# Kernel optimization log

Hardware: AMD Instinct MI355X
Metric: run time of the kernel (lower is better)

## Reference

```python
import jax, jax.numpy as jnp
import numpy as np

EMB = 256
HEADS = 4
HD = EMB // HEADS
BS, SZ = 4, 64


def _layernorm(x, g, b, eps=1e-5):
    mu = jnp.mean(x, axis=-1, keepdims=True)
    var = jnp.mean((x - mu) ** 2, axis=-1, keepdims=True)
    return (x - mu) * jax.lax.rsqrt(var + eps) * g + b


def setup_inputs() -> dict:
    key = jax.random.key(0)
    ks = jax.random.split(key, 12)
    s = lambda k, shape, sc: jax.random.normal(k, shape, jnp.float32) * sc
    return {
        "x": s(ks[0], (BS, EMB, SZ, SZ), 1.0),
        "ln1_g": jnp.ones((EMB,), jnp.float32),
        "ln1_b": jnp.zeros((EMB,), jnp.float32),
        "wq": s(ks[1], (HD, HD), HD ** -0.5), "bq": jnp.zeros((HD,), jnp.float32),
        "wk": s(ks[2], (HD, HD), HD ** -0.5), "bk": jnp.zeros((HD,), jnp.float32),
        "wv": s(ks[3], (HD, HD), HD ** -0.5), "bv": jnp.zeros((HD,), jnp.float32),
        "wo": s(ks[4], (EMB, EMB), EMB ** -0.5), "bo": jnp.zeros((EMB,), jnp.float32),
        "ln2_g": jnp.ones((EMB,), jnp.float32),
        "ln2_b": jnp.zeros((EMB,), jnp.float32),
        "w1": s(ks[5], (EMB, EMB), EMB ** -0.5), "b1": jnp.zeros((EMB,), jnp.float32),
        "w2": s(ks[6], (EMB, EMB), EMB ** -0.5), "b2": jnp.zeros((EMB,), jnp.float32),
    }


def reference(x, ln1_g, ln1_b, wq, bq, wk, bk, wv, bv, wo, bo, ln2_g, ln2_b, w1, b1, w2, b2):
    bs, c, sz, _ = x.shape
    seq = sz * sz
    xt = x.reshape(bs, c, seq).swapaxes(1, 2)  # [b, s, c]
    xn = _layernorm(xt, ln1_g, ln1_b)
    # split heads: [b, h, s, d]
    h = xn.reshape(bs, seq, HEADS, HD).transpose(0, 2, 1, 3)
    q = h @ wq + bq
    k = h @ wk + bk
    v = h @ wv + bv
    scores = jnp.einsum("bhqd,bhkd->bhqk", q, k) / (HD ** 0.5)
    attn = jax.nn.softmax(scores, axis=-1)
    o = jnp.einsum("bhqk,bhkd->bhqd", attn, v)
    o = o.transpose(0, 2, 1, 3).reshape(bs, seq, c)
    o = o @ wo + bo
    av = o + xt  # residual 1
    ff = _layernorm(av, ln2_g, ln2_b) @ w1 + b1
    ff = jax.nn.gelu(ff, approximate=False) @ w2 + b2
    out = ff + av  # residual 2
    return out.swapaxes(1, 2).reshape(bs, c, sz, sz)
```

## Files before the change

kernel.cpp:

```cpp
#include <hip/hip_runtime.h>
#include <hip/hip_bf16.h>
#include <cstdint>

typedef __attribute__((ext_vector_type(8))) short short8;
typedef __attribute__((ext_vector_type(4))) short short4_;
typedef __attribute__((ext_vector_type(4))) float float4_;

#define MFMA16(a,b,c)  __builtin_amdgcn_mfma_f32_16x16x32_bf16(a,b,c,0,0,0)
#define MFMA16K16(a,b,c) __builtin_amdgcn_mfma_f32_16x16x16bf16_1k(a,b,c,0,0,0)
#define EXP2(x) __builtin_amdgcn_exp2f(x)

__device__ __forceinline__ short f2bs(float f) {
    union { float f; uint32_t u; } c;
    c.f = f;
    c.u += 0x7FFF + ((c.u >> 16) & 1);
    return (short)(c.u >> 16);
}
__device__ __forceinline__ float s2f(short s) {
    union { uint32_t u; float f; } c;
    c.u = ((uint32_t)(uint16_t)s) << 16;
    return c.f;
}

static const int EMB = 256;
static const int SEQ = 4096;
static const int TOK = 16384;

#define QSCALE 0.18033688011112042f

__global__ __launch_bounds__(256) void repack_kernel(
    const float* wq, const float* wk, const float* wv,
    const float* wo, const float* w1, const float* w2,
    short* wqT, short* wkT, short* wvT, short* woT, short* w1T, short* w2T)
{
    int idx = blockIdx.x * 256 + threadIdx.x;
    if (idx < 3 * 4096) {
        int m = idx / 4096, r = idx % 4096;
        int n = r / 64, k = r % 64;
        const float* src = (m == 0) ? wq : (m == 1) ? wk : wv;
        short* dst = (m == 0) ? wqT : (m == 1) ? wkT : wvT;
        float v = src[k * 64 + n];
        if (m == 0) v *= QSCALE;
        dst[n * 64 + k] = f2bs(v);
    } else {
        int idx2 = idx - 3 * 4096;
        if (idx2 < 3 * 65536) {
            int m = idx2 / 65536, r = idx2 % 65536;
            int n = r / 256, k = r % 256;
            const float* src = (m == 0) ? wo : (m == 1) ? w1 : w2;
            short* dst = (m == 0) ? woT : (m == 1) ? w1T : w2T;
            dst[n * 256 + k] = f2bs(src[k * 256 + n]);
        }
    }
}

__global__ __launch_bounds__(64) void ln1_kernel(
    const float* x, const float* g, const float* bta,
    short* xn, short* xt)
{
    int t = blockIdx.x * 64 + threadIdx.x;
    int b = t >> 12, sp = t & 4095;
    const float* xb = x + (size_t)b * EMB * SEQ + sp;
    float sum = 0.f, ss = 0.f;
#pragma unroll 32
    for (int c = 0; c < 256; c++) {
        float v = xb[(size_t)c * SEQ];
        sum += v; ss += v * v;
    }
    float mu = sum * (1.f / 256.f);
    float var = ss * (1.f / 256.f) - mu * mu;
    float rs = rsqrtf(var + 1e-5f);
    short* xnr = xn + (size_t)t * 256;
    short* xtr = xt + (size_t)t * 256;
#pragma unroll 8
    for (int c = 0; c < 256; c += 4) {
        short4_ ra, na;
#pragma unroll
        for (int j = 0; j < 4; j++) {
            float v = xb[(size_t)(c + j) * SEQ];
            ra[j] = f2bs(v);
            na[j] = f2bs((v - mu) * rs * g[c + j] + bta[c + j]);
        }
        *(short4_*)(xtr + c) = ra;
        *(short4_*)(xnr + c) = na;
    }
}

__global__ __launch_bounds__(256) void qkv_kernel(
    const short* xn, const short* wqT, const short* wkT, const short* wvT,
    const float* bq, const float* bk, const float* bv,
    short* qo, short* ko, short* vto)
{
    int tid = threadIdx.x;
    int w = tid >> 6, lane = tid & 63, quad = lane >> 4, l15 = lane & 15;
    int m0 = blockIdx.x * 64 + w * 16;
    int row = m0 + l15;
    int bb = row >> 12;
    int s0 = (m0 & 4095) + quad * 4;

    short8 a0[4], a1[4];
#pragma unroll
    for (int h = 0; h < 4; h++) {
        a0[h] = *(const short8*)(xn + (size_t)row * 256 + h * 64 + quad * 8);
        a1[h] = *(const short8*)(xn + (size_t)row * 256 + h * 64 + 32 + quad * 8);
    }

#pragma unroll
    for (int p = 0; p < 3; p++) {
        const short* WT = (p == 0) ? wqT : (p == 1) ? wkT : wvT;
        const float* bias = (p == 0) ? bq : (p == 1) ? bk : bv;
        float bscale = (p == 0) ? QSCALE : 1.f;
#pragma unroll
        for (int nb = 0; nb < 4; nb++) {
            int col = nb * 16 + l15;
            short8 b0 = *(const short8*)(WT + col * 64 + quad * 8);
            short8 b1 = *(const short8*)(WT + col * 64 + 32 + quad * 8);
            float bvv = bias[col] * bscale;
#pragma unroll
            for (int h = 0; h < 4; h++) {
                float4_ acc = {bvv, bvv, bvv, bvv};
                acc = MFMA16(a0[h], b0, acc);
                acc = MFMA16(a1[h], b1, acc);
                size_t headbase = (size_t)(bb * 4 + h) * SEQ;
                if (p < 2) {
                    short* dst = (p == 0) ? qo : ko;
#pragma unroll
                    for (int r = 0; r < 4; r++)
                        dst[(headbase + s0 + r) * 64 + col] = f2bs(acc[r]);
                } else {
                    short4_ pk;
#pragma unroll
                    for (int r = 0; r < 4; r++) pk[r] = f2bs(acc[r]);
                    *(short4_*)(vto + ((size_t)(bb * 4 + h) * 64 + col) * SEQ + s0) = pk;
                }
            }
        }
    }
}

__global__ __launch_bounds__(256, 4) void flash_kernel(
    const short* q, const short* k, const short* vt,
    short* O0, short* O1, float* l0, float* l1)
{
    __shared__ short K_lds[64 * 64];
    __shared__ short V_lds[64 * 64];

    int tid = threadIdx.x;
    int w = tid >> 6, lane = tid & 63, quad = lane >> 4, l15 = lane & 15;
    int qt = blockIdx.x, bh = blockIdx.y, grp = blockIdx.z;
    int span = 64 / gridDim.z;

    const short* qb = q + (size_t)bh * SEQ * 64;
    const short* kb = k + (size_t)bh * SEQ * 64 + (size_t)grp * span * 64 * 64;
    const short* vb = vt + (size_t)bh * 64 * SEQ + grp * span * 64;

    int qrow0 = qt * 128 + w * 32 + l15;
    int qrow1 = qrow0 + 16;
    short8 qA0 = *(const short8*)(qb + (size_t)qrow0 * 64 + quad * 8);
    short8 qA1 = *(const short8*)(qb + (size_t)qrow0 * 64 + 32 + quad * 8);
    short8 qB0 = *(const short8*)(qb + (size_t)qrow1 * 64 + quad * 8);
    short8 qB1 = *(const short8*)(qb + (size_t)qrow1 * 64 + 32 + quad * 8);

    float4_ oacc0[4], oacc1[4];
#pragma unroll
    for (int md = 0; md < 4; md++) {
        oacc0[md] = {0.f, 0.f, 0.f, 0.f};
        oacc1[md] = {0.f, 0.f, 0.f, 0.f};
    }
    float li0 = 0.f, li1 = 0.f;

    int srow = tid >> 2;
    int sr7 = srow & 7;
    int c0 = tid & 3;
    int l7 = l15 & 7;

    int dcA = (c0 ^ sr7) << 3;
    int dcB = ((c0 + 4) ^ sr7) << 3;

    short8 kr0 = *(const short8*)(kb + (size_t)srow * 64 + c0 * 8);
    short8 kr1 = *(const short8*)(kb + (size_t)srow * 64 + (c0 + 4) * 8);
    short8 vr0 = *(const short8*)(vb + (size_t)srow * SEQ + c0 * 8);
    short8 vr1 = *(const short8*)(vb + (size_t)srow * SEQ + (c0 + 4) * 8);

    for (int kt = 0; kt < span; kt++) {
        __syncthreads();
        *(short8*)&K_lds[srow * 64 + dcA] = kr0;
        *(short8*)&K_lds[srow * 64 + dcB] = kr1;
        *(short8*)&V_lds[srow * 64 + dcA] = vr0;
        *(short8*)&V_lds[srow * 64 + dcB] = vr1;
        if (kt + 1 < span) {
            kr0 = *(const short8*)(kb + (size_t)((kt + 1) * 64 + srow) * 64 + c0 * 8);
            kr1 = *(const short8*)(kb + (size_t)((kt + 1) * 64 + srow) * 64 + (c0 + 4) * 8);
            vr0 = *(const short8*)(vb + (size_t)srow * SEQ + (kt + 1) * 64 + c0 * 8);
            vr1 = *(const short8*)(vb + (size_t)srow * SEQ + (kt + 1) * 64 + (c0 + 4) * 8);
        }
        asm volatile("s_waitcnt lgkmcnt(0)" ::: "memory");
        __builtin_amdgcn_s_barrier();
        asm volatile("" ::: "memory");

        float4_ s0[4], s1[4];
#pragma unroll
        for (int nb = 0; nb < 4; nb++) {
            short8 k0 = *(const short8*)&K_lds[(nb * 16 + l15) * 64 + ((quad ^ l7) << 3)];
            short8 k1 = *(const short8*)&K_lds[(nb * 16 + l15) * 64 + (((quad + 4) ^ l7) << 3)];
            float4_ a = {0.f, 0.f, 0.f, 0.f};
            a = MFMA16(k0, qA0, a);
            a = MFMA16(k1, qA1, a);
            s0[nb] = a;
            float4_ b = {0.f, 0.f, 0.f, 0.f};
            b = MFMA16(k0, qB0, b);
            b = MFMA16(k1, qB1, b);
            s1[nb] = b;
        }

        short4_ pf0[4], pf1[4];
#pragma unroll
        for (int nb = 0; nb < 4; nb++) {
            float p00 = EXP2(s0[nb][0]), p01 = EXP2(s0[nb][1]);
            float p02 = EXP2(s0[nb][2]), p03 = EXP2(s0[nb][3]);
            li0 += (p00 + p01) + (p02 + p03);
            float p10 = EXP2(s1[nb][0]), p11 = EXP2(s1[nb][1]);
            float p12 = EXP2(s1[nb][2]), p13 = EXP2(s1[nb][3]);
            li1 += (p10 + p11) + (p12 + p13);
            union { short4_ s; uint32_t u[2]; } pa, pb;
            asm("v_cvt_pk_bf16_f32 %0, %1, %2" : "=v"(pa.u[0]) : "v"(p00), "v"(p01));
            asm("v_cvt_pk_bf16_f32 %0, %1, %2" : "=v"(pa.u[1]) : "v"(p02), "v"(p03));
            asm("v_cvt_pk_bf16_f32 %0, %1, %2" : "=v"(pb.u[0]) : "v"(p10), "v"(p11));
            asm("v_cvt_pk_bf16_f32 %0, %1, %2" : "=v"(pb.u[1]) : "v"(p12), "v"(p13));
            pf0[nb] = pa.s;
            pf1[nb] = pb.s;
        }

#pragma unroll
        for (int md = 0; md < 4; md++)
#pragma unroll
            for (int nb = 0; nb < 4; nb++) {
                int c = nb * 2 + (quad >> 1);
                short4_ vf = *(const short4_*)&V_lds[(md * 16 + l15) * 64 +
                                                     ((c ^ l7) << 3) + ((quad & 1) << 2)];
                oacc0[md] = MFMA16K16(vf, pf0[nb], oacc0[md]);
                oacc1[md] = MFMA16K16(vf, pf1[nb], oacc1[md]);
            }
    }

    li0 += __shfl_xor(li0, 16);
    li0 += __shfl_xor(li0, 32);
    li1 += __shfl_xor(li1, 16);
    li1 += __shfl_xor(li1, 32);

    short* Op = grp ? O1 : O0;
    float* lp = grp ? l1 : l0;
    if (quad == 0) {
        lp[bh * 4096 + qrow0] = li0;
        lp[bh * 4096 + qrow1] = li1;
    }

    size_t ob0 = ((size_t)bh * 4096 + qrow0) * 64;
    size_t ob1 = ((size_t)bh * 4096 + qrow1) * 64;
#pragma unroll
    for (int md = 0; md < 4; md++) {
        short4_ pk0, pk1;
#pragma unroll
        for (int r = 0; r < 4; r++) {
            pk0[r] = f2bs(oacc0[md][r]);
            pk1[r] = f2bs(oacc1[md][r]);
        }
        *(short4_*)(Op + ob0 + md * 16 + quad * 4) = pk0;
        *(short4_*)(Op + ob1 + md * 16 + quad * 4) = pk1;
    }
}

__global__ __launch_bounds__(256) void combine_kernel(
    const short* O0, const short* O1, const float* l0, const float* l1,
    short* Oout, int two)
{
    int g = blockIdx.x * 256 + threadIdx.x;
    int qi = g >> 4;
    short4_ a = *(const short4_*)(O0 + (size_t)g * 4);
    float l = l0[qi];
    float4_ acc = {s2f(a[0]), s2f(a[1]), s2f(a[2]), s2f(a[3])};
    if (two) {
        short4_ b = *(const short4_*)(O1 + (size_t)g * 4);
        l += l1[qi];
#pragma unroll
        for (int j = 0; j < 4; j++) acc[j] += s2f(b[j]);
    }
    float inv = 1.f / l;
    short4_ pk;
#pragma unroll
    for (int j = 0; j < 4; j++) pk[j] = f2bs(acc[j] * inv);
    *(short4_*)(Oout + (size_t)g * 4) = pk;
}

__global__ __launch_bounds__(256) void mlp_kernel(
    const short* O,
    const short* woT, const short* w1T, const short* w2T,
    const float* bo, const float* b1, const float* b2,
    const float* g2, const float* be2,
    const short* xt, float* outf)
{
    __shared__ __align__(16) char smem[3 * 8448 + 128];
    short* av = (short*)smem;
    short* x2 = (short*)(smem + 8448);
    short* ff = (short*)(smem + 16896);
    float* stats = (float*)(smem + 25344);
    float* T = (float*)smem;

    int tid = threadIdx.x;
    int w = tid >> 6, lane = tid & 63, quad = lane >> 4, l15 = lane & 15;
    int m0 = blockIdx.x * 16;
    int n0 = w * 64;
    int arow = m0 + l15;
    int bbA = arow >> 12, spA = arow & 4095;

    float4_ acc[4];
#pragma unroll
    for (int nb = 0; nb < 4; nb++) {
        float bvv = bo[n0 + nb * 16 + l15];
        acc[nb] = {bvv, bvv, bvv, bvv};
    }
    for (int kc = 0; kc < 8; kc++) {
        int h = kc >> 1;
        int off = (kc & 1) * 32 + quad * 8;
        short8 a = *(const short8*)(O + ((size_t)(bbA * 4 + h) * 4096 + spA) * 64 + off);
#pragma unroll
        for (int nb = 0; nb < 4; nb++) {
            short8 b = *(const short8*)(woT + (size_t)(n0 + nb * 16 + l15) * 256 + kc * 32 + quad * 8);
            acc[nb] = MFMA16(a, b, acc[nb]);
        }
    }
#pragma unroll
    for (int nb = 0; nb < 4; nb++) {
        int col = n0 + nb * 16 + l15;
#pragma unroll
        for (int r = 0; r < 4; r++) {
            size_t t = (size_t)m0 + quad * 4 + r;
            av[(quad * 4 + r) * 264 + col] = f2bs(acc[nb][r] + s2f(xt[t * 256 + col]));
        }
    }
    __syncthreads();

    {
        int row = tid >> 4, sub = tid & 15;
        float sum = 0.f, ss = 0.f;
        short8 v0 = *(const short8*)&av[row * 264 + sub * 16];
        short8 v1 = *(const short8*)&av[row * 264 + sub * 16 + 8];
#pragma unroll
        for (int j = 0; j < 8; j++) {
            float a = s2f(v0[j]), b = s2f(v1[j]);
            sum += a + b; ss += a * a + b * b;
        }
#pragma unroll
        for (int off = 1; off < 16; off <<= 1) {
            sum += __shfl_xor(sum, off);
            ss += __shfl_xor(ss, off);
        }
        if (sub == 0) {
            float mu = sum * (1.f / 256.f);
            float var = ss * (1.f / 256.f) - mu * mu;
            stats[row] = mu;
            stats[16 + row] = rsqrtf(var + 1e-5f);
        }
    }
    __syncthreads();

    {
        int row = tid >> 4, sub = tid & 15;
        float mu = stats[row], rs = stats[16 + row];
#pragma unroll
        for (int j = 0; j < 16; j += 4) {
            int c = sub * 16 + j;
            short4_ rv = *(const short4_*)&av[row * 264 + c];
            short4_ pk;
#pragma unroll
            for (int i = 0; i < 4; i++)
                pk[i] = f2bs((s2f(rv[i]) - mu) * rs * g2[c + i] + be2[c + i]);
            *(short4_*)&x2[row * 264 + c] = pk;
        }
    }
    __syncthreads();

#pragma unroll
    for (int nb = 0; nb < 4; nb++) {
        float bvv = b1[n0 + nb * 16 + l15];
        acc[nb] = {bvv, bvv, bvv, bvv};
    }
    for (int kc = 0; kc < 8; kc++) {
        short8 a = *(const short8*)&x2[l15 * 264 + kc * 32 + quad * 8];
#pragma unroll
        for (int nb = 0; nb < 4; nb++) {
            short8 b = *(const short8*)(w1T + (size_t)(n0 + nb * 16 + l15) * 256 + kc * 32 + quad * 8);
            acc[nb] = MFMA16(a, b, acc[nb]);
        }
    }
#pragma unroll
    for (int nb = 0; nb < 4; nb++) {
        int col = n0 + nb * 16 + l15;
#pragma unroll
        for (int r = 0; r < 4; r++) {
            float v = acc[nb][r];
            v = 0.5f * v * (1.f + erff(v * 0.70710678118f));
            ff[(quad * 4 + r) * 264 + col] = f2bs(v);
        }
    }
    __syncthreads();

#pragma unroll
    for (int nb = 0; nb < 4; nb++) {
        float bvv = b2[n0 + nb * 16 + l15];
        acc[nb] = {bvv, bvv, bvv, bvv};
    }
    for (int kc = 0; kc < 8; kc++) {
        short8 a = *(const short8*)&ff[l15 * 264 + kc * 32 + quad * 8];
#pragma unroll
        for (int nb = 0; nb < 4; nb++) {
            short8 b = *(const short8*)(w2T + (size_t)(n0 + nb * 16 + l15) * 256 + kc * 32 + quad * 8);
            acc[nb] = MFMA16(a, b, acc[nb]);
        }
    }
    float vout[4][4];
#pragma unroll
    for (int nb = 0; nb < 4; nb++) {
        int col = n0 + nb * 16 + l15;
#pragma unroll
        for (int r = 0; r < 4; r++)
            vout[nb][r] = acc[nb][r] + s2f(av[(quad * 4 + r) * 264 + col]);
    }
    __syncthreads();

    float* tw = T + w * 1040;
#pragma unroll
    for (int nb = 0; nb < 4; nb++)
#pragma unroll
        for (int r = 0; r < 4; r++)
            tw[(quad * 4 + r) * 65 + nb * 16 + l15] = vout[nb][r];

    int bb = m0 >> 12;
    int spb = m0 & 4095;
    float* dst = outf + ((size_t)bb * 256 + n0 + lane) * SEQ + spb;
#pragma unroll
    for (int j = 0; j < 16; j += 4) {
        float4_ pk = {tw[(j + 0) * 65 + lane], tw[(j + 1) * 65 + lane],
                      tw[(j + 2) * 65 + lane], tw[(j + 3) * 65 + lane]};
        *(float4_*)(dst + j) = pk;
    }
}

extern "C" void kernel_launch(void* const* d_in, const int* in_sizes, int n_in,
                              void* d_out, int out_size, void* d_ws, size_t ws_size,
                              hipStream_t stream)
{
    const float* x     = (const float*)d_in[0];
    const float* ln1_g = (const float*)d_in[1];
    const float* ln1_b = (const float*)d_in[2];
    const float* wq    = (const float*)d_in[3];
    const float* bq    = (const float*)d_in[4];
    const float* wk    = (const float*)d_in[5];
    const float* bk    = (const float*)d_in[6];
    const float* wv    = (const float*)d_in[7];
    const float* bv    = (const float*)d_in[8];
    const float* wo    = (const float*)d_in[9];
    const float* bo    = (const float*)d_in[10];
    const float* ln2_g = (const float*)d_in[11];
    const float* ln2_b = (const float*)d_in[12];
    const float* w1    = (const float*)d_in[13];
    const float* b1    = (const float*)d_in[14];
    const float* w2    = (const float*)d_in[15];
    const float* b2    = (const float*)d_in[16];

    char* ws = (char*)d_ws;
    const size_t SZ_BF = (size_t)TOK * 256 * 2;

    short* wqT = (short*)(ws + 0);
    short* wkT = (short*)(ws + 8192);
    short* wvT = (short*)(ws + 16384);
    short* woT = (short*)(ws + 24576);
    short* w1T = (short*)(ws + 155648);
    short* w2T = (short*)(ws + 286720);
    char* base = ws + 524288;

    short* xt  = (short*)(base);
    short* kbuf= (short*)(base + SZ_BF);
    short* vtb = (short*)(base + 2 * SZ_BF);
    float* l0  = (float*)(base + 3 * SZ_BF);
    float* l1  = (float*)(base + 3 * SZ_BF + 262144);
    short* O1  = (short*)(base + 3 * SZ_BF + 524288);

    const size_t NEED_SPLIT = 524288 + 3 * SZ_BF + 524288 + SZ_BF;
    int nz = (ws_size >= NEED_SPLIT) ? 2 : 1;

    short* qb  = (short*)d_out;
    short* xn  = (short*)((char*)d_out + SZ_BF);
    short* O0  = xn;
    short* Onrm= vtb;

    repack_kernel<<<816, 256, 0, stream>>>(wq, wk, wv, wo, w1, w2,
                                           wqT, wkT, wvT, woT, w1T, w2T);
    ln1_kernel<<<TOK / 64, 64, 0, stream>>>(x, ln1_g, ln1_b, xn, xt);
    qkv_kernel<<<TOK / 64, 256, 0, stream>>>(xn, wqT, wkT, wvT, bq, bk, bv,
                                             qb, kbuf, vtb);
    flash_kernel<<<dim3(32, 16, nz), 256, 0, stream>>>(qb, kbuf, vtb, O0, O1, l0, l1);
    combine_kernel<<<4096, 256, 0, stream>>>(O0, O1, l0, l1, Onrm, nz - 1);
    mlp_kernel<<<TOK / 16, 256, 0, stream>>>(Onrm, woT, w1T, w2T, bo, b1, b2,
                                             ln2_g, ln2_b, xt, (float*)d_out);
}
```

Measured before the change: 288.9 us.

## Fuse split-KV combine into MLP prologue and interleave softmax with QK MFMAs

The separate combine kernel is removed when the workspace is large enough. The MLP kernel now reads both partial attention outputs and their row sums, normalizes them, and packs the result to bf16 inline before the Wo GEMM. This drops one launch and one round trip of the normalized output through memory, at the cost of extra loads and ALU work in the MLP prologue. The flash kernel also computes exp right after each score MFMA pair instead of in a separate loop, uses explicit waves-per-EU attributes, and raises wave priority around the PV MFMA loop.

New measurement: 280.3 us. 1.03x faster.

```diff
diff --git a/kernel.cpp b/kernel.cpp
--- a/kernel.cpp
+++ b/kernel.cpp
@@ -138,7 +138,9 @@
     }
 }
 
-__global__ __launch_bounds__(256, 4) void flash_kernel(
+__global__ __attribute__((amdgpu_flat_work_group_size(256, 256),
+                          amdgpu_waves_per_eu(4, 4)))
+void flash_kernel(
     const short* q, const short* k, const short* vt,
     short* O0, short* O1, float* l0, float* l1)
 {
@@ -198,7 +200,7 @@
         __builtin_amdgcn_s_barrier();
         asm volatile("" ::: "memory");
 
-        float4_ s0[4], s1[4];
+        short4_ pf0[4], pf1[4];
 #pragma unroll
         for (int nb = 0; nb < 4; nb++) {
             short8 k0 = *(const short8*)&K_lds[(nb * 16 + l15) * 64 + ((quad ^ l7) << 3)];
@@ -206,21 +208,15 @@
             float4_ a = {0.f, 0.f, 0.f, 0.f};
             a = MFMA16(k0, qA0, a);
             a = MFMA16(k1, qA1, a);
-            s0[nb] = a;
             float4_ b = {0.f, 0.f, 0.f, 0.f};
             b = MFMA16(k0, qB0, b);
             b = MFMA16(k1, qB1, b);
-            s1[nb] = b;
-        }
-
-        short4_ pf0[4], pf1[4];
-#pragma unroll
-        for (int nb = 0; nb < 4; nb++) {
-            float p00 = EXP2(s0[nb][0]), p01 = EXP2(s0[nb][1]);
-            float p02 = EXP2(s0[nb][2]), p03 = EXP2(s0[nb][3]);
+
+            float p00 = EXP2(a[0]), p01 = EXP2(a[1]);
+            float p02 = EXP2(a[2]), p03 = EXP2(a[3]);
             li0 += (p00 + p01) + (p02 + p03);
-            float p10 = EXP2(s1[nb][0]), p11 = EXP2(s1[nb][1]);
-            float p12 = EXP2(s1[nb][2]), p13 = EXP2(s1[nb][3]);
+            float p10 = EXP2(b[0]), p11 = EXP2(b[1]);
+            float p12 = EXP2(b[2]), p13 = EXP2(b[3]);
             li1 += (p10 + p11) + (p12 + p13);
             union { short4_ s; uint32_t u[2]; } pa, pb;
             asm("v_cvt_pk_bf16_f32 %0, %1, %2" : "=v"(pa.u[0]) : "v"(p00), "v"(p01));
@@ -231,6 +227,7 @@
             pf1[nb] = pb.s;
         }
 
+        __builtin_amdgcn_s_setprio(1);
 #pragma unroll
         for (int md = 0; md < 4; md++)
 #pragma unroll
@@ -241,6 +238,7 @@
                 oacc0[md] = MFMA16K16(vf, pf0[nb], oacc0[md]);
                 oacc1[md] = MFMA16K16(vf, pf1[nb], oacc1[md]);
             }
+        __builtin_amdgcn_s_setprio(0);
     }
 
     li0 += __shfl_xor(li0, 16);
@@ -293,7 +291,7 @@
 }
 
 __global__ __launch_bounds__(256) void mlp_kernel(
-    const short* O,
+    const short* O0, const short* O1, const float* l0, const float* l1, int two,
     const short* woT, const short* w1T, const short* w2T,
     const float* bo, const float* b1, const float* b2,
     const float* g2, const float* be2,
@@ -313,6 +311,15 @@
     int arow = m0 + l15;
     int bbA = arow >> 12, spA = arow & 4095;
 
+    float invh[4];
+    if (two) {
+#pragma unroll
+        for (int h = 0; h < 4; h++) {
+            size_t li = (size_t)(bbA * 4 + h) * 4096 + spA;
+            invh[h] = 1.f / (l0[li] + l1[li]);
+        }
+    }
+
     float4_ acc[4];
 #pragma unroll
     for (int nb = 0; nb < 4; nb++) {
@@ -322,7 +329,23 @@
     for (int kc = 0; kc < 8; kc++) {
         int h = kc >> 1;
         int off = (kc & 1) * 32 + quad * 8;
-        short8 a = *(const short8*)(O + ((size_t)(bbA * 4 + h) * 4096 + spA) * 64 + off);
+        size_t obase = ((size_t)(bbA * 4 + h) * 4096 + spA) * 64 + off;
+        short8 a;
+        if (two) {
+            short8 a0v = *(const short8*)(O0 + obase);
+            short8 a1v = *(const short8*)(O1 + obase);
+            float iv = invh[h];
+            union { short8 s; uint32_t u[4]; } pa;
+#pragma unroll
+            for (int jj = 0; jj < 4; jj++) {
+                float f0 = (s2f(a0v[2 * jj]) + s2f(a1v[2 * jj])) * iv;
+                float f1 = (s2f(a0v[2 * jj + 1]) + s2f(a1v[2 * jj + 1])) * iv;
+                asm("v_cvt_pk_bf16_f32 %0, %1, %2" : "=v"(pa.u[jj]) : "v"(f0), "v"(f1));
+            }
+            a = pa.s;
+        } else {
+            a = *(const short8*)(O0 + obase);
+        }
 #pragma unroll
         for (int nb = 0; nb < 4; nb++) {
             short8 b = *(const short8*)(woT + (size_t)(n0 + nb * 16 + l15) * 256 + kc * 32 + quad * 8);
@@ -485,13 +508,16 @@
     float* l0  = (float*)(base + 3 * SZ_BF);
     float* l1  = (float*)(base + 3 * SZ_BF + 262144);
     short* O1  = (short*)(base + 3 * SZ_BF + 524288);
+    short* O0w = (short*)(base + 4 * SZ_BF + 524288);
 
     const size_t NEED_SPLIT = 524288 + 3 * SZ_BF + 524288 + SZ_BF;
+    const size_t NEED_FUSED = 524288 + 5 * SZ_BF + 524288;
     int nz = (ws_size >= NEED_SPLIT) ? 2 : 1;
+    int fuse = (nz == 2 && ws_size >= NEED_FUSED);
 
     short* qb  = (short*)d_out;
     short* xn  = (short*)((char*)d_out + SZ_BF);
-    short* O0  = xn;
+    short* O0  = fuse ? O0w : xn;
     short* Onrm= vtb;
 
     repack_kernel<<<816, 256, 0, stream>>>(wq, wk, wv, wo, w1, w2,
@@ -500,7 +526,14 @@
     qkv_kernel<<<TOK / 64, 256, 0, stream>>>(xn, wqT, wkT, wvT, bq, bk, bv,
                                              qb, kbuf, vtb);
     flash_kernel<<<dim3(32, 16, nz), 256, 0, stream>>>(qb, kbuf, vtb, O0, O1, l0, l1);
-    combine_kernel<<<4096, 256, 0, stream>>>(O0, O1, l0, l1, Onrm, nz - 1);
-    mlp_kernel<<<TOK / 16, 256, 0, stream>>>(Onrm, woT, w1T, w2T, bo, b1, b2,
-                                             ln2_g, ln2_b, xt, (float*)d_out);
-}
+    if (fuse) {
+        mlp_kernel<<<TOK / 16, 256, 0, stream>>>(O0, O1, l0, l1, 2,
+                                                 woT, w1T, w2T, bo, b1, b2,
+                                                 ln2_g, ln2_b, xt, (float*)d_out);
+    } else {
+        combine_kernel<<<4096, 256, 0, stream>>>(O0, O1, l0, l1, Onrm, nz - 1);
+        mlp_kernel<<<TOK / 16, 256, 0, stream>>>(Onrm, O1, l0, l1, 0,
+                                                 woT, w1T, w2T, bo, b1, b2,
+                                                 ln2_g, ln2_b, xt, (float*)d_out);
+    }
+}
```
